# Performance work log

Measured on AMD Instinct MI355X. Metric: run time of the kernel, lower is better.

The kernel has to match this reference:

```python
import jax, jax.numpy as jnp
import numpy as np


def setup_inputs() -> dict:
    key = jax.random.key(0)
    k1, k2, k3, k4 = jax.random.split(key, 4)
    B, S, D_IN, D_OUT = 4, 4096, 2048, 2048
    x = jax.random.normal(k1, (B, S, D_IN), dtype=jnp.float32)
    weight = jax.random.normal(k2, (D_OUT, D_IN), dtype=jnp.float32) * 0.02
    scale_weight = jax.random.uniform(k3, (D_OUT,), dtype=jnp.float32, minval=0.5, maxval=1.5)
    bias = jax.random.normal(k4, (D_OUT,), dtype=jnp.float32) * 0.02
    return {"x": x, "weight": weight, "scale_weight": scale_weight, "bias": bias}


def reference(x, weight, scale_weight, bias):
    # FPScaledLinear.forward: cast weight to compute dtype, apply per-out-feature
    # scale (scale_weight viewed as [out, 1]), then F.linear(x, w, b).
    w = weight * scale_weight[:, None]            # [out, in]
    out = jnp.einsum('bsi,oi->bso', x, w) + bias  # [B, S, out]
    return out
```

## Files before the change

### kernel.cpp

```cpp
#include <hip/hip_runtime.h>

typedef __attribute__((ext_vector_type(8))) __bf16 bf16x8;
typedef __attribute__((ext_vector_type(4))) float f32x4;
typedef __attribute__((ext_vector_type(8))) unsigned short ushort8;
typedef const __attribute__((address_space(1))) unsigned int gq_t;
typedef __attribute__((address_space(3))) unsigned int lq_t;

__device__ __forceinline__ unsigned short f2bf(float f) {
  unsigned int u = __builtin_bit_cast(unsigned int, f);
  u += 0x7fffu + ((u >> 16) & 1u);
  return (unsigned short)(u >> 16);
}

__global__ void cvt_xw_kernel(const float* __restrict__ x, const float* __restrict__ w,
                              const float* __restrict__ scale,
                              ushort8* __restrict__ xa, ushort8* __restrict__ wb,
                              int n8x, int n8w, int k8) {
  int stride = gridDim.x * blockDim.x;
  int total = n8x + n8w;
  for (int i = blockIdx.x * blockDim.x + threadIdx.x; i < total; i += stride) {
    if (i < n8x) {
      const float4* p = (const float4*)(x) + 2 * (size_t)i;
      float4 v0 = p[0], v1 = p[1];
      ushort8 r;
      r[0] = f2bf(v0.x); r[1] = f2bf(v0.y); r[2] = f2bf(v0.z); r[3] = f2bf(v0.w);
      r[4] = f2bf(v1.x); r[5] = f2bf(v1.y); r[6] = f2bf(v1.z); r[7] = f2bf(v1.w);
      xa[i] = r;
    } else {
      int j = i - n8x;
      float s = scale[j / k8];
      const float4* p = (const float4*)(w) + 2 * (size_t)j;
      float4 v0 = p[0], v1 = p[1];
      ushort8 r;
      r[0] = f2bf(v0.x * s); r[1] = f2bf(v0.y * s); r[2] = f2bf(v0.z * s); r[3] = f2bf(v0.w * s);
      r[4] = f2bf(v1.x * s); r[5] = f2bf(v1.y * s); r[6] = f2bf(v1.z * s); r[7] = f2bf(v1.w * s);
      wb[j] = r;
    }
  }
}


#define BARRIER asm volatile("s_barrier" ::: "memory")
#define WAITV4 asm volatile("s_waitcnt vmcnt(4)" ::: "memory")
#define WAITV0 asm volatile("s_waitcnt vmcnt(0)" ::: "memory")
#define GL(p, d) __builtin_amdgcn_global_load_lds((gq_t*)(p), (lq_t*)(d), 16, 0, 0)

#define QUAD(MH, BG, NHB)                                                                \
  do {                                                                                   \
    __builtin_amdgcn_s_setprio(1);                                                       \
    _Pragma("unroll") for (int k_ = 0; k_ < 2; ++k_) {                                   \
      _Pragma("unroll") for (int mm = 0; mm < 4; ++mm) {                                 \
        _Pragma("unroll") for (int nn = 0; nn < 2; ++nn) {                               \
          acc[(MH)*4 + mm][(NHB)*2 + nn] = __builtin_amdgcn_mfma_f32_16x16x32_bf16(      \
              af[mm][k_], BG[nn][k_], acc[(MH)*4 + mm][(NHB)*2 + nn], 0, 0, 0);          \
        }                                                                                \
      }                                                                                  \
    }                                                                                    \
    __builtin_amdgcn_s_setprio(0);                                                       \
  } while (0)

#define TILE_BODY(T, CB)                                                                 \
  do {                                                                                   \
    const int t_ = (T);                                                                  \
    char* cur = lds + (CB) * 65536;                                                      \
    char* oth = lds + (((CB) ^ 1)) * 65536;                                              \
                 \
    LDA(cur, 0);                                                                         \
    LDB1(cur);                                                                           \
    if (t_ + 1 < NT) { GL(bP0lo, oth + 32768 + dstT);                                    \
                       GL(bP0hi, oth + 32768 + 8192 + dstT); }                           \
    BARRIER; QUAD(0, bg0, 0);                                                            \
                   \
    if (t_ + 1 < NT) { GL(aP1lo, oth + 16384 + dstT);                                    \
                       GL(aP1hi, oth + 16384 + 8192 + dstT); }                           \
    BARRIER; QUAD(0, bg1, 1);                                                            \
                                   \
    LDA(cur, 1);                                                                         \
    if (t_ + 2 < NT) { GL(aP0lo, cur + dstT);                                            \
                       GL(aP0hi, cur + 8192 + dstT); }                                   \
    BARRIER; QUAD(1, bg1, 1);                                                            \
       \
    if (t_ + 2 < NT) { GL(bP1lo, cur + 49152 + dstT);                                    \
                       GL(bP1hi, cur + 49152 + 8192 + dstT); }                           \
    if (t_ == NT - 2) { WAITV0; } else { WAITV4; }                                       \
    BARRIER; QUAD(1, bg0, 0);                                                            \
    if (t_ + 1 < NT) LDB0(oth);                                                          \
    aP0lo += 64; aP0hi += 64; aP1lo += 64; aP1hi += 64;                                  \
    bP0lo += 64; bP0hi += 64; bP1lo += 64; bP1hi += 64;                                  \
  } while (0)

__global__ __launch_bounds__(512, 2) void gemm256_8ph(
    const unsigned short* __restrict__ A, const unsigned short* __restrict__ B,
    const float* __restrict__ bias, float* __restrict__ C, int M, int N, int K) {
  extern __shared__ char lds[];

  const int nbn = N >> 8;
  const int nwg = (M >> 8) * nbn;
  int bid = blockIdx.x;
  if ((nwg & 7) == 0) {
    int q = nwg >> 3;
    bid = (bid & 7) * q + (bid >> 3);
  }
  const int bm = (bid / nbn) << 8;
  const int bn = (bid % nbn) << 8;

  const int tid = threadIdx.x;
  const int lane = tid & 63;
  const int wid = tid >> 6;
  const int wr = wid >> 2;
  const int wc = wid & 3;
  const int NT = K >> 6;
  const int dstT = tid * 16;

  const int colel = (((tid & 7) ^ ((tid >> 3) & 7)) << 3);
  const unsigned short* aBase = A + (size_t)(bm + (tid >> 3)) * K + colel;
  const unsigned short* bBase = B + (size_t)(bn + ((tid >> 8) << 6) + ((tid >> 3) & 31)) * K + colel;
  const unsigned short* aP0lo = aBase;
  const unsigned short* aP0hi = aBase + (size_t)128 * K;
  const unsigned short* aP1lo = aBase + (size_t)64 * K;
  const unsigned short* aP1hi = aBase + (size_t)192 * K;
  const unsigned short* bP0lo = bBase;
  const unsigned short* bP0hi = bBase + (size_t)128 * K;
  const unsigned short* bP1lo = bBase + (size_t)32 * K;
  const unsigned short* bP1hi = bBase + (size_t)160 * K;

  const int i15 = lane & 15;
  const int qg = lane >> 4;
  const int swz = (lane & 7) << 4;
  const int colp0 = (qg << 4) ^ swz;
  const int colp1 = ((qg << 4) | 64) ^ swz;
  const int aoff = wr * 8192 + i15 * 128;
  const int boff = 32768 + wc * 4096 + i15 * 128;

  f32x4 acc[8][4];
#pragma unroll
  for (int m = 0; m < 8; ++m)
#pragma unroll
    for (int n = 0; n < 4; ++n) acc[m][n] = (f32x4){0.f, 0.f, 0.f, 0.f};

  bf16x8 af[4][2];
  bf16x8 bg0[2][2];
  bf16x8 bg1[2][2];

  auto LDA = [&](const char* base, int mh) {
    const char* p = base + mh * 16384 + aoff;
#pragma unroll
    for (int mm = 0; mm < 4; ++mm) {
      af[mm][0] = *(const bf16x8*)(p + mm * 2048 + colp0);
      af[mm][1] = *(const bf16x8*)(p + mm * 2048 + colp1);
    }
  };
  auto LDB0 = [&](const char* base) {
    const char* p = base + boff;
#pragma unroll
    for (int nn = 0; nn < 2; ++nn) {
      bg0[nn][0] = *(const bf16x8*)(p + nn * 2048 + colp0);
      bg0[nn][1] = *(const bf16x8*)(p + nn * 2048 + colp1);
    }
  };
  auto LDB1 = [&](const char* base) {
    const char* p = base + 16384 + boff;
#pragma unroll
    for (int nn = 0; nn < 2; ++nn) {
      bg1[nn][0] = *(const bf16x8*)(p + nn * 2048 + colp0);
      bg1[nn][1] = *(const bf16x8*)(p + nn * 2048 + colp1);
    }
  };

  GL(aP0lo, lds + dstT);                     GL(aP0hi, lds + 8192 + dstT);
  GL(bP1lo, lds + 49152 + dstT);             GL(bP1hi, lds + 49152 + 8192 + dstT);
  GL(bP0lo, lds + 32768 + dstT);             GL(bP0hi, lds + 32768 + 8192 + dstT);
  GL(aP1lo, lds + 16384 + dstT);             GL(aP1hi, lds + 16384 + 8192 + dstT);
  GL(aP0lo + 64, lds + 65536 + dstT);        GL(aP0hi + 64, lds + 65536 + 8192 + dstT);
  GL(bP1lo + 64, lds + 65536 + 49152 + dstT);
  GL(bP1hi + 64, lds + 65536 + 49152 + 8192 + dstT);
  WAITV4;
  BARRIER;
  LDB0(lds);
  bP0lo += 64;  bP0hi += 64;  aP1lo += 64;  aP1hi += 64;
  aP0lo += 128; aP0hi += 128; bP1lo += 128; bP1hi += 128;

  for (int t = 0; t < NT; t += 2) {
    TILE_BODY(t, 0);
    TILE_BODY(t + 1, 1);
  }

  const int r0 = bm + wr * 128 + ((lane >> 4) << 2);
  const int c0 = bn + wc * 64 + (lane & 15);
  float bv[4];
#pragma unroll
  for (int n = 0; n < 4; ++n) bv[n] = bias[c0 + n * 16];
#pragma unroll
  for (int m = 0; m < 8; ++m) {
#pragma unroll
    for (int r = 0; r < 4; ++r) {
      float* crow = C + (size_t)(r0 + m * 16 + r) * N + c0;
#pragma unroll
      for (int n = 0; n < 4; ++n) crow[n * 16] = acc[m][n][r] + bv[n];
    }
  }
}

__global__ void gemm_fallback_kernel(const float* __restrict__ X, const float* __restrict__ W,
                                     const float* __restrict__ scale, const float* __restrict__ bias,
                                     float* __restrict__ out, int M, int N, int K) {
  __shared__ float as[64][33];
  __shared__ float bs[64][33];
  int tx = threadIdx.x & 15, ty = threadIdx.x >> 4;
  int brow = blockIdx.y * 64, bcol = blockIdx.x * 64;
  float acc[4][4] = {};
  for (int k0 = 0; k0 < K; k0 += 32) {
    int kw = (K - k0 < 32) ? (K - k0) : 32;
    for (int i = 0; i < 8; ++i) {
      int idx = (int)threadIdx.x + i * 256;
      int r = idx >> 5, c = idx & 31;
      int ga = brow + r, gb = bcol + r;
      as[r][c] = (ga < M && c < kw) ? X[(size_t)ga * K + k0 + c] : 0.f;
      bs[r][c] = (gb < N && c < kw) ? W[(size_t)gb * K + k0 + c] * scale[gb] : 0.f;
    }
    __syncthreads();
    for (int k = 0; k < 32; ++k)
#pragma unroll
      for (int i = 0; i < 4; ++i)
#pragma unroll
        for (int j = 0; j < 4; ++j)
          acc[i][j] += as[ty * 4 + i][k] * bs[tx * 4 + j][k];
    __syncthreads();
  }
  for (int i = 0; i < 4; ++i) {
    int r = brow + ty * 4 + i;
    if (r >= M) continue;
    for (int j = 0; j < 4; ++j) {
      int c = bcol + tx * 4 + j;
      if (c < N) out[(size_t)r * N + c] = acc[i][j] + bias[c];
    }
  }
}

extern "C" void kernel_launch(void* const* d_in, const int* in_sizes, int n_in,
                              void* d_out, int out_size, void* d_ws, size_t ws_size,
                              hipStream_t stream) {
  const float* x     = (const float*)d_in[0];
  const float* w     = (const float*)d_in[1];
  const float* scale = (const float*)d_in[2];
  const float* bias  = (const float*)d_in[3];
  float* out = (float*)d_out;

  const long N = in_sizes[2];
  const long K = in_sizes[1] / N;
  const long M = (long)in_sizes[0] / K;

  const size_t need = ((size_t)M * K + (size_t)N * K) * sizeof(unsigned short);
  const long NT = K / 64;
  const bool ok = (ws_size >= need) && (M % 256 == 0) && (N % 256 == 0) &&
                  (K % 128 == 0) && (NT >= 4);

  if (ok) {
    unsigned short* xa = (unsigned short*)d_ws;
    unsigned short* wb = xa + (size_t)M * K;
    int n8x = (int)((size_t)M * K / 8);
    int n8w = (int)((size_t)N * K / 8);
    cvt_xw_kernel<<<2048, 256, 0, stream>>>(x, w, scale, (ushort8*)xa, (ushort8*)wb,
                                            n8x, n8w, (int)(K / 8));

    (void)hipFuncSetAttribute((const void*)gemm256_8ph,
                              hipFuncAttributeMaxDynamicSharedMemorySize, 131072);
    int nwg = (int)((M / 256) * (N / 256));
    gemm256_8ph<<<nwg, 512, 131072, stream>>>(xa, wb, bias, out, (int)M, (int)N, (int)K);
  } else {
    dim3 grid((unsigned)((N + 63) / 64), (unsigned)((M + 63) / 64));
    gemm_fallback_kernel<<<grid, 256, 0, stream>>>(x, w, scale, bias, out, (int)M, (int)N, (int)K);
  }
}
```

Measured before the change: 199.3 us.

## Split 256x256 GEMM tile across 16 waves instead of 8

Moves the bf16 MFMA GEMM from 512 threads (8 waves, 128x64 per wave) to 1024 threads (16 waves, 64x64 per wave) over the same 256x256 tile and LDS layout. Each thread now issues one global-to-LDS load per half-tile instead of two, and the vmcnt waits and prologue are adjusted to match. The goal is more waves to hide latency and less register pressure per wave. The cost is more LDS reads per MFMA, since each wave reuses its fragments less, and barriers that now span 16 waves. Launch bounds (1024,4) together with 128KB of LDS still allow only one workgroup per CU.

Result: slower. 263.2 us (+32.0%).

```diff
diff --git a/kernel.cpp b/kernel.cpp
--- a/kernel.cpp
+++ b/kernel.cpp
@@ -41,7 +41,7 @@
 
 
 #define BARRIER asm volatile("s_barrier" ::: "memory")
-#define WAITV4 asm volatile("s_waitcnt vmcnt(4)" ::: "memory")
+#define WAITV1 asm volatile("s_waitcnt vmcnt(1)" ::: "memory")
 #define WAITV0 asm volatile("s_waitcnt vmcnt(0)" ::: "memory")
 #define GL(p, d) __builtin_amdgcn_global_load_lds((gq_t*)(p), (lq_t*)(d), 16, 0, 0)
 
@@ -49,10 +49,10 @@
   do {                                                                                   \
     __builtin_amdgcn_s_setprio(1);                                                       \
     _Pragma("unroll") for (int k_ = 0; k_ < 2; ++k_) {                                   \
-      _Pragma("unroll") for (int mm = 0; mm < 4; ++mm) {                                 \
+      _Pragma("unroll") for (int mm = 0; mm < 2; ++mm) {                                 \
         _Pragma("unroll") for (int nn = 0; nn < 2; ++nn) {                               \
-          acc[(MH)*4 + mm][(NHB)*2 + nn] = __builtin_amdgcn_mfma_f32_16x16x32_bf16(      \
-              af[mm][k_], BG[nn][k_], acc[(MH)*4 + mm][(NHB)*2 + nn], 0, 0, 0);          \
+          acc[(MH)*2 + mm][(NHB)*2 + nn] = __builtin_amdgcn_mfma_f32_16x16x32_bf16(      \
+              af[mm][k_], BG[nn][k_], acc[(MH)*2 + mm][(NHB)*2 + nn], 0, 0, 0);          \
         }                                                                                \
       }                                                                                  \
     }                                                                                    \
@@ -64,32 +64,26 @@
     const int t_ = (T);                                                                  \
     char* cur = lds + (CB) * 65536;                                                      \
     char* oth = lds + (((CB) ^ 1)) * 65536;                                              \
-                 \
+                                \
     LDA(cur, 0);                                                                         \
+    if (t_ + 1 < NT) GL(bP0, oth + 32768 + dstT);                                        \
+    BARRIER; QUAD(0, bg0, 0);                                                            \
+                                \
     LDB1(cur);                                                                           \
-    if (t_ + 1 < NT) { GL(bP0lo, oth + 32768 + dstT);                                    \
-                       GL(bP0hi, oth + 32768 + 8192 + dstT); }                           \
-    BARRIER; QUAD(0, bg0, 0);                                                            \
-                   \
-    if (t_ + 1 < NT) { GL(aP1lo, oth + 16384 + dstT);                                    \
-                       GL(aP1hi, oth + 16384 + 8192 + dstT); }                           \
+    if (t_ + 1 < NT) { GL(aP0, oth + dstT); GL(aP1, oth + 16384 + dstT); }               \
     BARRIER; QUAD(0, bg1, 1);                                                            \
-                                   \
+                                                                \
     LDA(cur, 1);                                                                         \
-    if (t_ + 2 < NT) { GL(aP0lo, cur + dstT);                                            \
-                       GL(aP0hi, cur + 8192 + dstT); }                                   \
     BARRIER; QUAD(1, bg1, 1);                                                            \
-       \
-    if (t_ + 2 < NT) { GL(bP1lo, cur + 49152 + dstT);                                    \
-                       GL(bP1hi, cur + 49152 + 8192 + dstT); }                           \
-    if (t_ == NT - 2) { WAITV0; } else { WAITV4; }                                       \
+                \
+    if (t_ + 2 < NT) GL(bP1, cur + 49152 + dstT);                                        \
+    if (t_ < NT - 2) { WAITV1; } else { WAITV0; }                                        \
     BARRIER; QUAD(1, bg0, 0);                                                            \
     if (t_ + 1 < NT) LDB0(oth);                                                          \
-    aP0lo += 64; aP0hi += 64; aP1lo += 64; aP1hi += 64;                                  \
-    bP0lo += 64; bP0hi += 64; bP1lo += 64; bP1hi += 64;                                  \
+    aP0 += 64; aP1 += 64; bP0 += 64; bP1 += 64;                                          \
   } while (0)
 
-__global__ __launch_bounds__(512, 2) void gemm256_8ph(
+__global__ __launch_bounds__(1024, 4) void gemm256_16w(
     const unsigned short* __restrict__ A, const unsigned short* __restrict__ B,
     const float* __restrict__ bias, float* __restrict__ C, int M, int N, int K) {
   extern __shared__ char lds[];
@@ -113,39 +107,33 @@
   const int dstT = tid * 16;
 
   const int colel = (((tid & 7) ^ ((tid >> 3) & 7)) << 3);
-  const unsigned short* aBase = A + (size_t)(bm + (tid >> 3)) * K + colel;
-  const unsigned short* bBase = B + (size_t)(bn + ((tid >> 8) << 6) + ((tid >> 3) & 31)) * K + colel;
-  const unsigned short* aP0lo = aBase;
-  const unsigned short* aP0hi = aBase + (size_t)128 * K;
-  const unsigned short* aP1lo = aBase + (size_t)64 * K;
-  const unsigned short* aP1hi = aBase + (size_t)192 * K;
-  const unsigned short* bP0lo = bBase;
-  const unsigned short* bP0hi = bBase + (size_t)128 * K;
-  const unsigned short* bP1lo = bBase + (size_t)32 * K;
-  const unsigned short* bP1hi = bBase + (size_t)160 * K;
+  const unsigned short* aP0 = A + (size_t)(bm + (tid >> 3)) * K + colel;
+  const unsigned short* aP1 = aP0 + (size_t)128 * K;
+  const unsigned short* bP0 = B + (size_t)(bn + (tid >> 3)) * K + colel;
+  const unsigned short* bP1 = bP0 + (size_t)128 * K;
 
   const int i15 = lane & 15;
   const int qg = lane >> 4;
   const int swz = (lane & 7) << 4;
   const int colp0 = (qg << 4) ^ swz;
   const int colp1 = ((qg << 4) | 64) ^ swz;
-  const int aoff = wr * 8192 + i15 * 128;
-  const int boff = 32768 + wc * 4096 + i15 * 128;
-
-  f32x4 acc[8][4];
-#pragma unroll
-  for (int m = 0; m < 8; ++m)
+  const int aoff = (wr >> 1) * 16384 + (wr & 1) * 8192 + i15 * 128;
+  const int boff = 32768 + (wc >> 1) * 16384 + (wc & 1) * 8192 + i15 * 128;
+
+  f32x4 acc[4][4];
+#pragma unroll
+  for (int m = 0; m < 4; ++m)
 #pragma unroll
     for (int n = 0; n < 4; ++n) acc[m][n] = (f32x4){0.f, 0.f, 0.f, 0.f};
 
-  bf16x8 af[4][2];
+  bf16x8 af[2][2];
   bf16x8 bg0[2][2];
   bf16x8 bg1[2][2];
 
   auto LDA = [&](const char* base, int mh) {
-    const char* p = base + mh * 16384 + aoff;
-#pragma unroll
-    for (int mm = 0; mm < 4; ++mm) {
+    const char* p = base + aoff + mh * 4096;
+#pragma unroll
+    for (int mm = 0; mm < 2; ++mm) {
       af[mm][0] = *(const bf16x8*)(p + mm * 2048 + colp0);
       af[mm][1] = *(const bf16x8*)(p + mm * 2048 + colp1);
     }
@@ -159,7 +147,7 @@
     }
   };
   auto LDB1 = [&](const char* base) {
-    const char* p = base + 16384 + boff;
+    const char* p = base + boff + 4096;
 #pragma unroll
     for (int nn = 0; nn < 2; ++nn) {
       bg1[nn][0] = *(const bf16x8*)(p + nn * 2048 + colp0);
@@ -167,31 +155,29 @@
     }
   };
 
-  GL(aP0lo, lds + dstT);                     GL(aP0hi, lds + 8192 + dstT);
-  GL(bP1lo, lds + 49152 + dstT);             GL(bP1hi, lds + 49152 + 8192 + dstT);
-  GL(bP0lo, lds + 32768 + dstT);             GL(bP0hi, lds + 32768 + 8192 + dstT);
-  GL(aP1lo, lds + 16384 + dstT);             GL(aP1hi, lds + 16384 + 8192 + dstT);
-  GL(aP0lo + 64, lds + 65536 + dstT);        GL(aP0hi + 64, lds + 65536 + 8192 + dstT);
-  GL(bP1lo + 64, lds + 65536 + 49152 + dstT);
-  GL(bP1hi + 64, lds + 65536 + 49152 + 8192 + dstT);
-  WAITV4;
+  GL(aP0, lds + dstT);
+  GL(bP0, lds + 32768 + dstT);
+  GL(bP1, lds + 49152 + dstT);
+  GL(aP1, lds + 16384 + dstT);
+  GL(bP1 + 64, lds + 65536 + 49152 + dstT);
+  WAITV1;
   BARRIER;
   LDB0(lds);
-  bP0lo += 64;  bP0hi += 64;  aP1lo += 64;  aP1hi += 64;
-  aP0lo += 128; aP0hi += 128; bP1lo += 128; bP1hi += 128;
+  bP0 += 64; aP0 += 64; aP1 += 64;
+  bP1 += 128;
 
   for (int t = 0; t < NT; t += 2) {
     TILE_BODY(t, 0);
     TILE_BODY(t + 1, 1);
   }
 
-  const int r0 = bm + wr * 128 + ((lane >> 4) << 2);
+  const int r0 = bm + wr * 64 + ((lane >> 4) << 2);
   const int c0 = bn + wc * 64 + (lane & 15);
   float bv[4];
 #pragma unroll
   for (int n = 0; n < 4; ++n) bv[n] = bias[c0 + n * 16];
 #pragma unroll
-  for (int m = 0; m < 8; ++m) {
+  for (int m = 0; m < 4; ++m) {
 #pragma unroll
     for (int r = 0; r < 4; ++r) {
       float* crow = C + (size_t)(r0 + m * 16 + r) * N + c0;
@@ -263,10 +249,10 @@
     cvt_xw_kernel<<<2048, 256, 0, stream>>>(x, w, scale, (ushort8*)xa, (ushort8*)wb,
                                             n8x, n8w, (int)(K / 8));
 
-    (void)hipFuncSetAttribute((const void*)gemm256_8ph,
+    (void)hipFuncSetAttribute((const void*)gemm256_16w,
                               hipFuncAttributeMaxDynamicSharedMemorySize, 131072);
     int nwg = (int)((M / 256) * (N / 256));
-    gemm256_8ph<<<nwg, 512, 131072, stream>>>(xa, wb, bias, out, (int)M, (int)N, (int)K);
+    gemm256_16w<<<nwg, 1024, 131072, stream>>>(xa, wb, bias, out, (int)M, (int)N, (int)K);
   } else {
     dim3 grid((unsigned)((N + 63) / 64), (unsigned)((M + 63) / 64));
     gemm_fallback_kernel<<<grid, 256, 0, stream>>>(x, w, scale, bias, out, (int)M, (int)N, (int)K);
```
